# Performance work log

Measured on AMD Instinct MI355X. Metric: run time of the kernel, lower is better.

## Reference

```python
import jax, jax.numpy as jnp
import numpy as np

N_HEADS = 16


def setup_inputs() -> dict:
    key = jax.random.key(0)
    k_x, k_len, k_pos, k_attn, k_proj = jax.random.split(key, 5)
    B, W, c, C = 4, 256, 32, 1024
    x = jax.random.normal(k_x, (B, W, c, C), dtype=jnp.float32)
    # ragged word lengths in [1, c]; left-aligned padding mask as in pad()
    lengths = jax.random.randint(k_len, (B, W), 1, c + 1)
    attention_mask = (jnp.arange(c)[None, None, :] < lengths[:, :, None]).astype(jnp.int32)
    pos_emb = jax.random.normal(k_pos, (W, C), dtype=jnp.float32) * 0.02
    attn_w = jax.random.normal(k_attn, (C, 3 * C), dtype=jnp.float32) * (C ** -0.5)
    proj_w = jax.random.normal(k_proj, (C, C), dtype=jnp.float32) * (C ** -0.5)
    return {"x": x, "attention_mask": attention_mask, "pos_emb": pos_emb,
            "attn_w": attn_w, "proj_w": proj_w}


def reference(x, attention_mask, pos_emb, attn_w, proj_w):
    # first_time=True path of CharAttention.forward (eval mode: dropout = identity)
    B, W, c, C = x.shape
    H = N_HEADS
    hd = C // H
    last_ix = jnp.sum(attention_mask, axis=2) - 1          # [B, W]

    qkv = jnp.einsum('bwce,ef->bwcf', x, attn_w)            # [B, W, c, 3C]
    q, k, v = jnp.split(qkv, 3, axis=-1)
    # [B, W, c, C] -> [B, W, H, c, hd]
    def to_heads(t):
        return t.reshape(B, W, c, H, hd).transpose(0, 1, 3, 2, 4)
    q, k, v = to_heads(q), to_heads(k), to_heads(v)

    scale = 1.0 / jnp.sqrt(jnp.asarray(hd, dtype=x.dtype))
    scores = jnp.einsum('bwhqd,bwhkd->bwhqk', q, k) * scale  # [B, W, H, c, c]
    causal = jnp.tril(jnp.ones((c, c), dtype=bool))
    scores = jnp.where(causal[None, None, None], scores, jnp.finfo(x.dtype).min)
    attn = jax.nn.softmax(scores, axis=-1)
    o = jnp.einsum('bwhqk,bwhkd->bwhqd', attn, v)            # [B, W, H, c, hd]
    o = o.transpose(0, 1, 3, 2, 4).reshape(B, W, c, C)       # [B, W, c, C]

    # gather the last real-character position of each word
    idx = last_ix[:, :, None, None]                          # [B, W, 1, 1]
    gathered = jnp.take_along_axis(o, idx, axis=2)[:, :, 0, :]  # [B, W, C]

    out = gathered + pos_emb[None, :, :]
    out = jnp.einsum('bwe,ef->bwf', out, proj_w)
    return out
```

## Files before the change

### kernel.cpp

```cpp
#include <hip/hip_runtime.h>
#include <hip/hip_bf16.h>
#include <stdint.h>

typedef __attribute__((ext_vector_type(8))) short short8;
typedef __attribute__((ext_vector_type(4))) float floatx4;

#define GPTR(p) (const __attribute__((address_space(1))) void*)(p)
#define LPTR(p) (__attribute__((address_space(3))) void*)(p)

__device__ __forceinline__ ushort f2bf(float f) {
    union { float f; uint32_t u; } v; v.f = f;
    uint32_t u = v.u;
    uint32_t r = (u + 0x7FFFu + ((u >> 16) & 1u)) >> 16;
    return (ushort)r;
}
__device__ __forceinline__ float bf2f(ushort b) {
    union { uint32_t u; float f; } v; v.u = ((uint32_t)b) << 16;
    return v.f;
}

__global__ void qrow_kernel(const float* __restrict__ x, const int* __restrict__ mask,
                            ushort* __restrict__ xq) {
    __shared__ int t_sh;
    int bw = blockIdx.x, tid = threadIdx.x;
    if (tid < 32) {
        int s = mask[bw * 32 + tid];
        #pragma unroll
        for (int off = 16; off; off >>= 1) s += __shfl_xor(s, off);
        if (tid == 0) t_sh = s - 1;
    }
    __syncthreads();
    int t = t_sh;
    const float4* src = (const float4*)(x + ((size_t)bw * 32 + t) * 1024);
    float4 v = src[tid];
    ushort4 o;
    o.x = f2bf(v.x); o.y = f2bf(v.y); o.z = f2bf(v.z); o.w = f2bf(v.w);
    ((ushort4*)(xq + (size_t)bw * 1024))[tid] = o;
}

__global__ void wcvt_kernel(const float* __restrict__ attn_w, const float* __restrict__ proj_w,
                            ushort* __restrict__ wqT, ushort* __restrict__ wk,
                            ushort* __restrict__ wvT, ushort* __restrict__ wpT) {
    __shared__ float tile[32][33];
    int bx = blockIdx.x;
    int r0 = blockIdx.y * 32;
    int tx = threadIdx.x, ty = threadIdx.y;
    if (bx >= 96) {
        int c0 = (bx - 96) * 32;
        for (int i = ty; i < 32; i += 8)
            wk[(size_t)(r0 + i) * 1024 + c0 + tx] =
                f2bf(attn_w[(size_t)(r0 + i) * 3072 + 1024 + c0 + tx]);
        return;
    }
    const float* src; ushort* dst; int N, csrc0, c0;
    if (bx < 32)      { src = attn_w; dst = wqT; N = 3072; c0 = bx * 32;        csrc0 = c0; }
    else if (bx < 64) { src = attn_w; dst = wvT; N = 3072; c0 = (bx - 32) * 32; csrc0 = 2048 + c0; }
    else              { src = proj_w; dst = wpT; N = 1024; c0 = (bx - 64) * 32; csrc0 = c0; }
    for (int i = ty; i < 32; i += 8)
        tile[i][tx] = src[(size_t)(r0 + i) * N + csrc0 + tx];
    __syncthreads();
    for (int i = ty; i < 32; i += 8)
        dst[(size_t)(c0 + i) * 1024 + r0 + tx] = f2bf(tile[tx][i]);
}

__global__ __launch_bounds__(256)
void gemm64sk_kernel(const ushort* __restrict__ A, const ushort* __restrict__ Bt,
                     float* __restrict__ Cpart) {
    __shared__ ushort As[64 * 32];
    __shared__ ushort Bs[64 * 32];

    const int bm = blockIdx.x, bn = blockIdx.y, z = blockIdx.z;
    const int kofs = z * 256;

    const int tid  = threadIdx.x;
    const int wave = tid >> 6;
    const int lane = tid & 63;
    const int wm = wave & 1, wn = wave >> 1;
    const int quad = lane >> 4, l15 = lane & 15;

    floatx4 acc[2][2] = {};

    const int srow = wave * 16 + (lane >> 2);
    const int kcol = (lane & 3) * 8;

    for (int kt = 0; kt < 256; kt += 32) {
        const ushort* gA = A  + (size_t)(bm * 64 + srow) * 1024 + kofs + kt + kcol;
        const ushort* gB = Bt + (size_t)(bn * 64 + srow) * 1024 + kofs + kt + kcol;
        ushort* lA = As + (wave * 16) * 32;
        ushort* lB = Bs + (wave * 16) * 32;
        __builtin_amdgcn_global_load_lds(GPTR(gA), LPTR(lA), 16, 0, 0);
        __builtin_amdgcn_global_load_lds(GPTR(gB), LPTR(lB), 16, 0, 0);
        __syncthreads();

        short8 af[2], bf[2];
        #pragma unroll
        for (int i = 0; i < 2; ++i)
            af[i] = *(const short8*)&As[(wm * 32 + i * 16 + l15) * 32 + quad * 8];
        #pragma unroll
        for (int j = 0; j < 2; ++j)
            bf[j] = *(const short8*)&Bs[(wn * 32 + j * 16 + l15) * 32 + quad * 8];
        #pragma unroll
        for (int i = 0; i < 2; ++i)
            #pragma unroll
            for (int j = 0; j < 2; ++j)
                acc[i][j] = __builtin_amdgcn_mfma_f32_16x16x32_bf16(af[i], bf[j], acc[i][j], 0, 0, 0);
        __syncthreads();
    }

    #pragma unroll
    for (int i = 0; i < 2; ++i) {
        #pragma unroll
        for (int j = 0; j < 2; ++j) {
            int r0 = bm * 64 + wm * 32 + i * 16 + quad * 4;
            int c  = bn * 64 + wn * 32 + j * 16 + l15;
            #pragma unroll
            for (int r = 0; r < 4; ++r)
                Cpart[(size_t)z * 1048576 + (size_t)(r0 + r) * 1024 + c] = acc[i][j][r];
        }
    }
}

template <bool OUT_BF16>
__global__ void combine4_kernel(const float* __restrict__ P, void* __restrict__ C) {
    int i = blockIdx.x * 256 + threadIdx.x;
    const float4* p = (const float4*)P;
    float4 a = p[i], b = p[i + 262144], c = p[i + 524288], d = p[i + 786432];
    float4 s;
    s.x = a.x + b.x + c.x + d.x;
    s.y = a.y + b.y + c.y + d.y;
    s.z = a.z + b.z + c.z + d.z;
    s.w = a.w + b.w + c.w + d.w;
    if (OUT_BF16) {
        ushort4 o;
        o.x = f2bf(s.x); o.y = f2bf(s.y); o.z = f2bf(s.z); o.w = f2bf(s.w);
        ((ushort4*)C)[i] = o;
    } else {
        ((float4*)C)[i] = s;
    }
}

template <bool OUT_BF16>
__global__ __launch_bounds__(256)
void gemm128_kernel(const ushort* __restrict__ A, int lda, long sA,
                    const ushort* __restrict__ Bt, int ldb, long sB,
                    void* __restrict__ C, int ldc, long sC, int K) {
    __shared__ ushort As[128 * 32];
    __shared__ ushort Bs[128 * 32];

    const int bm = blockIdx.x, bn = blockIdx.y, z = blockIdx.z;
    A  += (size_t)z * sA;
    Bt += (size_t)z * sB;

    const int tid  = threadIdx.x;
    const int wave = tid >> 6;
    const int lane = tid & 63;
    const int wm = wave & 1, wn = wave >> 1;
    const int quad = lane >> 4, l15 = lane & 15;

    floatx4 acc[4][4] = {};

    const int arow = bm * 128 + wave * 16 + (lane >> 2);
    const int brow = bn * 128 + wave * 16 + (lane >> 2);
    const int kcol = (lane & 3) * 8;

    for (int kt = 0; kt < K; kt += 32) {
        #pragma unroll
        for (int iss = 0; iss < 2; ++iss) {
            const ushort* gA = A  + (size_t)(arow + iss * 64) * lda + kt + kcol;
            const ushort* gB = Bt + (size_t)(brow + iss * 64) * ldb + kt + kcol;
            ushort* lA = As + (iss * 64 + wave * 16) * 32;
            ushort* lB = Bs + (iss * 64 + wave * 16) * 32;
            __builtin_amdgcn_global_load_lds(GPTR(gA), LPTR(lA), 16, 0, 0);
            __builtin_amdgcn_global_load_lds(GPTR(gB), LPTR(lB), 16, 0, 0);
        }
        __syncthreads();

        short8 af[4], bf[4];
        #pragma unroll
        for (int i = 0; i < 4; ++i)
            af[i] = *(const short8*)&As[(wm * 64 + i * 16 + l15) * 32 + quad * 8];
        #pragma unroll
        for (int j = 0; j < 4; ++j)
            bf[j] = *(const short8*)&Bs[(wn * 64 + j * 16 + l15) * 32 + quad * 8];
        #pragma unroll
        for (int i = 0; i < 4; ++i)
            #pragma unroll
            for (int j = 0; j < 4; ++j)
                acc[i][j] = __builtin_amdgcn_mfma_f32_16x16x32_bf16(af[i], bf[j], acc[i][j], 0, 0, 0);
        __syncthreads();
    }

    #pragma unroll
    for (int i = 0; i < 4; ++i) {
        #pragma unroll
        for (int j = 0; j < 4; ++j) {
            int r0 = bm * 128 + wm * 64 + i * 16 + quad * 4;
            int c  = bn * 128 + wn * 64 + j * 16 + l15;
            #pragma unroll
            for (int r = 0; r < 4; ++r) {
                float v = acc[i][j][r];
                size_t idx = (size_t)z * sC + (size_t)(r0 + r) * ldc + c;
                if (OUT_BF16) ((ushort*)C)[idx] = f2bf(v);
                else          ((float*) C)[idx] = v;
            }
        }
    }
}

template <bool OUT_BF16, bool ADD_POS>
__global__ __launch_bounds__(256)
void gemm64_kernel(const ushort* __restrict__ A, int lda, long sA,
                   const ushort* __restrict__ Bt, int ldb, long sB,
                   void* __restrict__ C, int ldc, int cColPerZ, int K,
                   const float* __restrict__ pos) {
    __shared__ ushort As[64 * 32];
    __shared__ ushort Bs[64 * 32];

    const int bm = blockIdx.x, bn = blockIdx.y, z = blockIdx.z;
    A  += (size_t)z * sA;
    Bt += (size_t)z * sB;

    const int tid  = threadIdx.x;
    const int wave = tid >> 6;
    const int lane = tid & 63;
    const int wm = wave & 1, wn = wave >> 1;
    const int quad = lane >> 4, l15 = lane & 15;

    floatx4 acc[2][2] = {};

    const int srow = wave * 16 + (lane >> 2);
    const int kcol = (lane & 3) * 8;

    for (int kt = 0; kt < K; kt += 32) {
        const ushort* gA = A  + (size_t)(bm * 64 + srow) * lda + kt + kcol;
        const ushort* gB = Bt + (size_t)(bn * 64 + srow) * ldb + kt + kcol;
        ushort* lA = As + (wave * 16) * 32;
        ushort* lB = Bs + (wave * 16) * 32;
        __builtin_amdgcn_global_load_lds(GPTR(gA), LPTR(lA), 16, 0, 0);
        __builtin_amdgcn_global_load_lds(GPTR(gB), LPTR(lB), 16, 0, 0);
        __syncthreads();

        short8 af[2], bf[2];
        #pragma unroll
        for (int i = 0; i < 2; ++i)
            af[i] = *(const short8*)&As[(wm * 32 + i * 16 + l15) * 32 + quad * 8];
        #pragma unroll
        for (int j = 0; j < 2; ++j)
            bf[j] = *(const short8*)&Bs[(wn * 32 + j * 16 + l15) * 32 + quad * 8];
        #pragma unroll
        for (int i = 0; i < 2; ++i)
            #pragma unroll
            for (int j = 0; j < 2; ++j)
                acc[i][j] = __builtin_amdgcn_mfma_f32_16x16x32_bf16(af[i], bf[j], acc[i][j], 0, 0, 0);
        __syncthreads();
    }

    #pragma unroll
    for (int i = 0; i < 2; ++i) {
        #pragma unroll
        for (int j = 0; j < 2; ++j) {
            int r0 = bm * 64 + wm * 32 + i * 16 + quad * 4;
            int cc = z * cColPerZ + bn * 64 + wn * 32 + j * 16 + l15;
            #pragma unroll
            for (int r = 0; r < 4; ++r) {
                float v = acc[i][j][r];
                if (ADD_POS) v += pos[(size_t)((r0 + r) & 255) * 1024 + cc];
                size_t idx = (size_t)(r0 + r) * ldc + cc;
                if (OUT_BF16) ((ushort*)C)[idx] = f2bf(v);
                else          ((float*) C)[idx] = v;
            }
        }
    }
}

__global__ __launch_bounds__(256)
void attn2_kernel(const float* __restrict__ x, const int* __restrict__ mask,
                  const ushort* __restrict__ U, ushort* __restrict__ Z) {
    __shared__ ushort Xs[32 * 1032];
    __shared__ ushort Us[16 * 1032];
    __shared__ float  Ss[16 * 33];
    __shared__ float  Ps[32 * 16];
    __shared__ int    t_sh;

    const int bw = blockIdx.x;
    const int tid = threadIdx.x;
    const int wave = tid >> 6, lane = tid & 63;
    const int quad = lane >> 4, l15 = lane & 15;

    if (tid < 32) {
        int s = mask[bw * 32 + tid];
        #pragma unroll
        for (int off = 16; off; off >>= 1) s += __shfl_xor(s, off);
        if (tid == 0) t_sh = s - 1;
    }
    __syncthreads();
    const int t = t_sh;

    const float4* xsrc = (const float4*)(x + (size_t)bw * 32 * 1024);
    int n4 = (t + 1) * 256;
    for (int i = tid; i < n4; i += 256) {
        float4 v = xsrc[i];
        int j = i >> 8, c4 = i & 255;
        ushort4 o; o.x = f2bf(v.x); o.y = f2bf(v.y); o.z = f2bf(v.z); o.w = f2bf(v.w);
        *(ushort4*)&Xs[j * 1032 + c4 * 4] = o;
    }
    const ushort* ubase = U + (size_t)bw * 16384;
    for (int i = tid; i < 16 * 128; i += 256) {
        int h = i >> 7, c = i & 127;
        *(short8*)&Us[h * 1032 + c * 8] = *(const short8*)&ubase[i * 8];
    }
    __syncthreads();

    if (wave < 2) {
        floatx4 acc = {0.f, 0.f, 0.f, 0.f};
        int arow = wave * 16 + l15;
        for (int kt = 0; kt < 1024; kt += 32) {
            short8 a = *(const short8*)&Xs[arow * 1032 + kt + quad * 8];
            short8 b = *(const short8*)&Us[l15  * 1032 + kt + quad * 8];
            acc = __builtin_amdgcn_mfma_f32_16x16x32_bf16(a, b, acc, 0, 0, 0);
        }
        #pragma unroll
        for (int r = 0; r < 4; ++r)
            Ss[l15 * 33 + wave * 16 + quad * 4 + r] = acc[r] * 0.125f;
    }
    __syncthreads();

    if (wave == 0) {
        float s[8]; float mx = -1e30f;
        #pragma unroll
        for (int r = 0; r < 8; ++r) {
            int j = quad * 8 + r;
            float v = Ss[l15 * 33 + j];
            v = (j <= t) ? v : -1e30f;
            s[r] = v; mx = fmaxf(mx, v);
        }
        mx = fmaxf(mx, __shfl_xor(mx, 16));
        mx = fmaxf(mx, __shfl_xor(mx, 32));
        float l = 0.f;
        #pragma unroll
        for (int r = 0; r < 8; ++r) { s[r] = __expf(s[r] - mx); l += s[r]; }
        l += __shfl_xor(l, 16);
        l += __shfl_xor(l, 32);
        float inv = 1.f / l;
        #pragma unroll
        for (int r = 0; r < 8; ++r)
            Ps[(quad * 8 + r) * 16 + l15] = s[r] * inv;
    }
    __syncthreads();

    float z[16][4];
    #pragma unroll
    for (int h = 0; h < 16; ++h)
        #pragma unroll
        for (int c = 0; c < 4; ++c) z[h][c] = 0.f;
    const int e0 = tid * 4;
    for (int j = 0; j <= t; ++j) {
        float4 p0 = *(const float4*)&Ps[j * 16 + 0];
        float4 p1 = *(const float4*)&Ps[j * 16 + 4];
        float4 p2 = *(const float4*)&Ps[j * 16 + 8];
        float4 p3 = *(const float4*)&Ps[j * 16 + 12];
        float pr[16] = {p0.x, p0.y, p0.z, p0.w, p1.x, p1.y, p1.z, p1.w,
                        p2.x, p2.y, p2.z, p2.w, p3.x, p3.y, p3.z, p3.w};
        ushort4 xv = *(const ushort4*)&Xs[j * 1032 + e0];
        float xf[4] = {bf2f(xv.x), bf2f(xv.y), bf2f(xv.z), bf2f(xv.w)};
        #pragma unroll
        for (int h = 0; h < 16; ++h)
            #pragma unroll
            for (int c = 0; c < 4; ++c)
                z[h][c] += pr[h] * xf[c];
    }
    #pragma unroll
    for (int h = 0; h < 16; ++h) {
        ushort4 o;
        o.x = f2bf(z[h][0]); o.y = f2bf(z[h][1]);
        o.z = f2bf(z[h][2]); o.w = f2bf(z[h][3]);
        *(ushort4*)&Z[(size_t)bw * 16384 + h * 1024 + e0] = o;
    }
}

extern "C" void kernel_launch(void* const* d_in, const int* in_sizes, int n_in,
                              void* d_out, int out_size, void* d_ws, size_t ws_size,
                              hipStream_t stream) {
    const float* x        = (const float*)d_in[0];
    const int*   mask     = (const int*)  d_in[1];
    const float* pos_emb  = (const float*)d_in[2];
    const float* attn_w   = (const float*)d_in[3];
    const float* proj_w   = (const float*)d_in[4];
    float*       out      = (float*)d_out;

    const long MB2 = 1048576;

    char* ws = (char*)d_ws;
    size_t off = 0;
    ushort* U_bf  = (ushort*)(ws + off); off += (size_t)16 * MB2 * 2;
    ushort* Z_bf  = (ushort*)(ws + off); off += (size_t)16 * MB2 * 2;
    float*  qpart = (float*) (ws + off); off += (size_t)4 * MB2 * 4;
    float*  opart = (float*) (ws + off); off += (size_t)4 * MB2 * 4;
    ushort* wqT   = (ushort*)(ws + off); off += MB2 * 2;
    ushort* wk    = (ushort*)(ws + off); off += MB2 * 2;
    ushort* wvT   = (ushort*)(ws + off); off += MB2 * 2;
    ushort* wpT   = (ushort*)(ws + off); off += MB2 * 2;
    ushort* xq_bf = (ushort*)(ws + off); off += MB2 * 2;
    ushort* q_bf  = (ushort*)(ws + off); off += MB2 * 2;
    ushort* y_bf  = (ushort*)(ws + off); off += MB2 * 2;

    qrow_kernel<<<1024, 256, 0, stream>>>(x, mask, xq_bf);

    wcvt_kernel<<<dim3(128, 32), dim3(32, 8), 0, stream>>>(attn_w, proj_w, wqT, wk, wvT, wpT);

    gemm64sk_kernel<<<dim3(16, 16, 4), 256, 0, stream>>>(xq_bf, wqT, qpart);
    combine4_kernel<true><<<1024, 256, 0, stream>>>(qpart, (void*)q_bf);

    gemm128_kernel<true><<<dim3(8, 8, 16), 256, 0, stream>>>(
        q_bf, 1024, 64, wk, 1024, 64, (void*)U_bf, 16384, 1024, 64);

    attn2_kernel<<<1024, 256, 0, stream>>>(x, mask, U_bf, Z_bf);

    gemm64_kernel<true, true><<<dim3(16, 1, 16), 256, 0, stream>>>(
        Z_bf, 16384, 1024, wvT, 1024, 65536, (void*)y_bf, 1024, 64, 1024, pos_emb);

    gemm64sk_kernel<<<dim3(16, 16, 4), 256, 0, stream>>>(y_bf, wpT, opart);
    combine4_kernel<false><<<1024, 256, 0, stream>>>(opart, (void*)out);
}
```

Before: 321.0 us.

## Chunk attention score GEMM over K to shrink LDS and merge prep kernels

The attention kernel now stages X and U in four 256-column chunks instead of holding full 1024-wide rows. This cuts LDS from roughly 100KB to about 25KB, so more blocks can be resident per CU. All four waves now run the score MFMAs, splitting the K dimension in halves and reducing partial sums through shared memory. The P·X accumulation rereads fp32 x from global memory rather than from LDS, and the qrow and weight-conversion kernels are fused into one launch. The cost is extra barriers and repeated global reads of x.

```diff
diff --git a/kernel.cpp b/kernel.cpp
--- a/kernel.cpp
+++ b/kernel.cpp
@@ -19,32 +19,35 @@
     return v.f;
 }
 
-__global__ void qrow_kernel(const float* __restrict__ x, const int* __restrict__ mask,
+__global__ void prep_kernel(const float* __restrict__ attn_w, const float* __restrict__ proj_w,
+                            const float* __restrict__ x, const int* __restrict__ mask,
+                            ushort* __restrict__ wqT, ushort* __restrict__ wk,
+                            ushort* __restrict__ wvT, ushort* __restrict__ wpT,
                             ushort* __restrict__ xq) {
+    __shared__ float tile[32][33];
     __shared__ int t_sh;
-    int bw = blockIdx.x, tid = threadIdx.x;
-    if (tid < 32) {
-        int s = mask[bw * 32 + tid];
-        #pragma unroll
-        for (int off = 16; off; off >>= 1) s += __shfl_xor(s, off);
-        if (tid == 0) t_sh = s - 1;
-    }
-    __syncthreads();
-    int t = t_sh;
-    const float4* src = (const float4*)(x + ((size_t)bw * 32 + t) * 1024);
-    float4 v = src[tid];
-    ushort4 o;
-    o.x = f2bf(v.x); o.y = f2bf(v.y); o.z = f2bf(v.z); o.w = f2bf(v.w);
-    ((ushort4*)(xq + (size_t)bw * 1024))[tid] = o;
-}
-
-__global__ void wcvt_kernel(const float* __restrict__ attn_w, const float* __restrict__ proj_w,
-                            ushort* __restrict__ wqT, ushort* __restrict__ wk,
-                            ushort* __restrict__ wvT, ushort* __restrict__ wpT) {
-    __shared__ float tile[32][33];
-    int bx = blockIdx.x;
-    int r0 = blockIdx.y * 32;
-    int tx = threadIdx.x, ty = threadIdx.y;
+    const int bx = blockIdx.x, by = blockIdx.y;
+    const int tid = threadIdx.x;
+
+    if (bx >= 128) {
+        int bw = (bx - 128) * 32 + by;
+        if (tid < 32) {
+            int s = mask[bw * 32 + tid];
+            #pragma unroll
+            for (int off = 16; off; off >>= 1) s += __shfl_xor(s, off);
+            if (tid == 0) t_sh = s - 1;
+        }
+        __syncthreads();
+        int t = t_sh;
+        float4 v = ((const float4*)(x + ((size_t)bw * 32 + t) * 1024))[tid];
+        ushort4 o;
+        o.x = f2bf(v.x); o.y = f2bf(v.y); o.z = f2bf(v.z); o.w = f2bf(v.w);
+        ((ushort4*)(xq + (size_t)bw * 1024))[tid] = o;
+        return;
+    }
+
+    const int tx = tid & 31, ty = tid >> 5;
+    const int r0 = by * 32;
     if (bx >= 96) {
         int c0 = (bx - 96) * 32;
         for (int i = ty; i < 32; i += 8)
@@ -276,9 +279,10 @@
 __global__ __launch_bounds__(256)
 void attn2_kernel(const float* __restrict__ x, const int* __restrict__ mask,
                   const ushort* __restrict__ U, ushort* __restrict__ Z) {
-    __shared__ ushort Xs[32 * 1032];
-    __shared__ ushort Us[16 * 1032];
-    __shared__ float  Ss[16 * 33];
+    __shared__ ushort Xs[32 * 264];
+    __shared__ ushort Us[16 * 264];
+    __shared__ float  Sp[2][16][16];
+    __shared__ float  Ss[16 * 36];
     __shared__ float  Ps[32 * 16];
     __shared__ int    t_sh;
 
@@ -296,32 +300,45 @@
     __syncthreads();
     const int t = t_sh;
 
-    const float4* xsrc = (const float4*)(x + (size_t)bw * 32 * 1024);
-    int n4 = (t + 1) * 256;
-    for (int i = tid; i < n4; i += 256) {
-        float4 v = xsrc[i];
-        int j = i >> 8, c4 = i & 255;
-        ushort4 o; o.x = f2bf(v.x); o.y = f2bf(v.y); o.z = f2bf(v.z); o.w = f2bf(v.w);
-        *(ushort4*)&Xs[j * 1032 + c4 * 4] = o;
-    }
+    const int m  = wave & 1;
+    const int kh = wave >> 1;
+    floatx4 acc = {0.f, 0.f, 0.f, 0.f};
+
+    const float4* xsrc = (const float4*)(x + (size_t)bw * 32768);
     const ushort* ubase = U + (size_t)bw * 16384;
-    for (int i = tid; i < 16 * 128; i += 256) {
-        int h = i >> 7, c = i & 127;
-        *(short8*)&Us[h * 1032 + c * 8] = *(const short8*)&ubase[i * 8];
+
+    for (int c = 0; c < 4; ++c) {
+        int nx4 = (t + 1) * 64;
+        for (int i = tid; i < nx4; i += 256) {
+            int j = i >> 6, c4 = i & 63;
+            float4 v = xsrc[j * 256 + c * 64 + c4];
+            ushort4 o; o.x = f2bf(v.x); o.y = f2bf(v.y); o.z = f2bf(v.z); o.w = f2bf(v.w);
+            *(ushort4*)&Xs[j * 264 + c4 * 4] = o;
+        }
+        for (int i = tid; i < 16 * 32; i += 256) {
+            int h = i >> 5, c8 = i & 31;
+            *(short8*)&Us[h * 264 + c8 * 8] = *(const short8*)&ubase[h * 1024 + c * 256 + c8 * 8];
+        }
+        __syncthreads();
+        #pragma unroll
+        for (int ks = 0; ks < 4; ++ks) {
+            short8 a = *(const short8*)&Xs[(m * 16 + l15) * 264 + kh * 128 + ks * 32 + quad * 8];
+            short8 b = *(const short8*)&Us[l15 * 264 + kh * 128 + ks * 32 + quad * 8];
+            acc = __builtin_amdgcn_mfma_f32_16x16x32_bf16(a, b, acc, 0, 0, 0);
+        }
+        __syncthreads();
+    }
+
+    if (kh == 1) {
+        #pragma unroll
+        for (int r = 0; r < 4; ++r) Sp[m][quad * 4 + r][l15] = acc[r];
     }
     __syncthreads();
-
-    if (wave < 2) {
-        floatx4 acc = {0.f, 0.f, 0.f, 0.f};
-        int arow = wave * 16 + l15;
-        for (int kt = 0; kt < 1024; kt += 32) {
-            short8 a = *(const short8*)&Xs[arow * 1032 + kt + quad * 8];
-            short8 b = *(const short8*)&Us[l15  * 1032 + kt + quad * 8];
-            acc = __builtin_amdgcn_mfma_f32_16x16x32_bf16(a, b, acc, 0, 0, 0);
-        }
+    if (kh == 0) {
         #pragma unroll
         for (int r = 0; r < 4; ++r)
-            Ss[l15 * 33 + wave * 16 + quad * 4 + r] = acc[r] * 0.125f;
+            Ss[l15 * 36 + m * 16 + quad * 4 + r] =
+                (acc[r] + Sp[m][quad * 4 + r][l15]) * 0.125f;
     }
     __syncthreads();
 
@@ -330,7 +347,7 @@
         #pragma unroll
         for (int r = 0; r < 8; ++r) {
             int j = quad * 8 + r;
-            float v = Ss[l15 * 33 + j];
+            float v = Ss[l15 * 36 + j];
             v = (j <= t) ? v : -1e30f;
             s[r] = v; mx = fmaxf(mx, v);
         }
@@ -352,8 +369,7 @@
     #pragma unroll
     for (int h = 0; h < 16; ++h)
         #pragma unroll
-        for (int c = 0; c < 4; ++c) z[h][c] = 0.f;
-    const int e0 = tid * 4;
+        for (int cc = 0; cc < 4; ++cc) z[h][cc] = 0.f;
     for (int j = 0; j <= t; ++j) {
         float4 p0 = *(const float4*)&Ps[j * 16 + 0];
         float4 p1 = *(const float4*)&Ps[j * 16 + 4];
@@ -361,14 +377,15 @@
         float4 p3 = *(const float4*)&Ps[j * 16 + 12];
         float pr[16] = {p0.x, p0.y, p0.z, p0.w, p1.x, p1.y, p1.z, p1.w,
                         p2.x, p2.y, p2.z, p2.w, p3.x, p3.y, p3.z, p3.w};
-        ushort4 xv = *(const ushort4*)&Xs[j * 1032 + e0];
-        float xf[4] = {bf2f(xv.x), bf2f(xv.y), bf2f(xv.z), bf2f(xv.w)};
+        float4 xv = xsrc[j * 256 + tid];
+        float xf[4] = {xv.x, xv.y, xv.z, xv.w};
         #pragma unroll
         for (int h = 0; h < 16; ++h)
             #pragma unroll
-            for (int c = 0; c < 4; ++c)
-                z[h][c] += pr[h] * xf[c];
-    }
+            for (int cc = 0; cc < 4; ++cc)
+                z[h][cc] += pr[h] * xf[cc];
+    }
+    const int e0 = tid * 4;
     #pragma unroll
     for (int h = 0; h < 16; ++h) {
         ushort4 o;
@@ -404,9 +421,8 @@
     ushort* q_bf  = (ushort*)(ws + off); off += MB2 * 2;
     ushort* y_bf  = (ushort*)(ws + off); off += MB2 * 2;
 
-    qrow_kernel<<<1024, 256, 0, stream>>>(x, mask, xq_bf);
-
-    wcvt_kernel<<<dim3(128, 32), dim3(32, 8), 0, stream>>>(attn_w, proj_w, wqT, wk, wvT, wpT);
+    prep_kernel<<<dim3(160, 32), 256, 0, stream>>>(attn_w, proj_w, x, mask,
+                                                   wqT, wk, wvT, wpT, xq_bf);
 
     gemm64sk_kernel<<<dim3(16, 16, 4), 256, 0, stream>>>(xq_bf, wqT, qpart);
     combine4_kernel<true><<<1024, 256, 0, stream>>>(qpart, (void*)q_bf);
```

Result: faster. 280.5 us (-12.6%).
